# Kernel tuning notes

Measured on AMD Instinct MI355X. Metric: run time of the kernel, lower is better.

Reference implementation:

```python
import jax, jax.numpy as jnp
import numpy as np


def setup_inputs() -> dict:
    key = jax.random.key(0)
    k1, k2 = jax.random.split(key)
    B, N_A, UNITS = 8192, 1024, 4096
    x = jax.random.normal(k1, (B, N_A), dtype=jnp.float32)
    # keras 'uniform' initializer is U(-0.05, 0.05)
    mu = jax.random.uniform(k2, (N_A, UNITS), dtype=jnp.float32, minval=-0.05, maxval=0.05)
    return {"x": x, "mu": mu, "gamma": 0.5}


def reference(x, mu, gamma):
    # Squared L2 distance from each row of x (B, n_a) to each codebook column
    # of mu (n_a, units), computed without materializing (B, n_a, units):
    x_sq = jnp.sum(x * x, axis=-1, keepdims=True)          # (B, 1)
    mu_sq = jnp.sum(mu * mu, axis=0, keepdims=True)        # (1, units)
    cross = jnp.einsum('bn,nu->bu', x, mu)                 # (B, units)
    l2 = x_sq + mu_sq - 2.0 * cross                        # (B, units)
    return jnp.exp(-gamma * l2)
```

## Files before the change

kernel.cpp:

```cpp
#include <hip/hip_runtime.h>

#define B_ROWS 8192
#define K_DIM  1024
#define N_COLS 4096

#define UNDERFLOW_T 120.0f

__global__ __launch_bounds__(256) void mu_norms_k(const float* __restrict__ mu,
                                                  float* __restrict__ pmax) {
  const int blk = blockIdx.x;
  const int tid = threadIdx.x;
  const int g  = blk & 63;
  const int kq = blk >> 6;
  const int tx = tid & 63;
  const int ty = tid >> 6;
  const int u  = g * 64 + tx;
  const int k0 = kq * 64 + ty * 16;
  float s = 0.f;
#pragma unroll
  for (int i = 0; i < 16; ++i) {
    const float v = mu[(size_t)(k0 + i) * N_COLS + u];
    s += v * v;
  }
  __shared__ float red[4][64];
  red[ty][tx] = s;
  __syncthreads();
  if (ty == 0) {
    float p = red[0][tx] + red[1][tx] + red[2][tx] + red[3][tx];
#pragma unroll
    for (int off = 32; off; off >>= 1) p = fmaxf(p, __shfl_down(p, off));
    if (tx == 0) pmax[blk] = p;
  }
}

__global__ __launch_bounds__(256) void main_k(const float* __restrict__ x,
                                              const float* __restrict__ mu,
                                              const float* __restrict__ gp,
                                              const float* __restrict__ pmax,
                                              float* __restrict__ out) {
  __shared__ float sh[4 * K_DIM];
  __shared__ float xs[4];
  __shared__ int   sflag;
  const int tid  = threadIdx.x;
  const int w    = tid >> 6;
  const int lane = tid & 63;
  const int r0   = blockIdx.x * 4;
  const float g  = gp[0];

  {
    const float4* xr =
        reinterpret_cast<const float4*>(x + (size_t)(r0 + w) * K_DIM);
    float4* sh4 = reinterpret_cast<float4*>(sh) + w * (K_DIM / 4);
    float s = 0.f;
#pragma unroll
    for (int i = 0; i < 4; ++i) {
      const float4 v = xr[lane + i * 64];
      sh4[lane + i * 64] = v;
      s += v.x * v.x + v.y * v.y + v.z * v.z + v.w * v.w;
    }
#pragma unroll
    for (int off = 32; off; off >>= 1) s += __shfl_down(s, off);
    if (lane == 0) xs[w] = s;
  }
  __syncthreads();

  if (tid < 64) {
    float sg = 0.f;
#pragma unroll
    for (int kq = 0; kq < 16; ++kq) sg += pmax[kq * 64 + tid];
#pragma unroll
    for (int off = 32; off; off >>= 1) sg = fmaxf(sg, __shfl_down(sg, off));
    if (tid == 0) {
      const float xmin2 = fminf(fminf(xs[0], xs[1]), fminf(xs[2], xs[3]));
      const float d = sqrtf(xmin2) - sqrtf(sg);
      sflag = (d > 0.f && g * d * d > UNDERFLOW_T) ? 1 : 0;
    }
  }
  __syncthreads();

  if (sflag) {
    const float4 z = {0.f, 0.f, 0.f, 0.f};
    float4* o = reinterpret_cast<float4*>(out + (size_t)r0 * N_COLS);
#pragma unroll
    for (int i = 0; i < 16; ++i) o[tid + i * 256] = z;
    return;
  }

  for (int c = 0; c < 16; ++c) {
    const int u = c * 256 + tid;
    float acc0 = 0.f, acc1 = 0.f, acc2 = 0.f, acc3 = 0.f, ms = 0.f;
    for (int k = 0; k < K_DIM; ++k) {
      const float mv = mu[(size_t)k * N_COLS + u];
      ms   += mv * mv;
      acc0 += sh[0 * K_DIM + k] * mv;
      acc1 += sh[1 * K_DIM + k] * mv;
      acc2 += sh[2 * K_DIM + k] * mv;
      acc3 += sh[3 * K_DIM + k] * mv;
    }
    out[(size_t)(r0 + 0) * N_COLS + u] = expf(-g * (xs[0] + ms - 2.f * acc0));
    out[(size_t)(r0 + 1) * N_COLS + u] = expf(-g * (xs[1] + ms - 2.f * acc1));
    out[(size_t)(r0 + 2) * N_COLS + u] = expf(-g * (xs[2] + ms - 2.f * acc2));
    out[(size_t)(r0 + 3) * N_COLS + u] = expf(-g * (xs[3] + ms - 2.f * acc3));
  }
}

__global__ __launch_bounds__(256) void rbf_naive(const float* __restrict__ x,
                                                 const float* __restrict__ mu,
                                                 const float* __restrict__ gp,
                                                 float* __restrict__ out) {
  const int u = blockIdx.x * 256 + threadIdx.x;
  const int b = blockIdx.y;
  const float* xr = x + (size_t)b * K_DIM;
  float dot = 0.f, xsv = 0.f, ms = 0.f;
  for (int k = 0; k < K_DIM; ++k) {
    const float xv = xr[k];
    const float mv = mu[(size_t)k * N_COLS + u];
    dot += xv * mv; xsv += xv * xv; ms += mv * mv;
  }
  out[(size_t)b * N_COLS + u] = __expf(-gp[0] * (xsv + ms - 2.f * dot));
}

extern "C" void kernel_launch(void* const* d_in, const int* in_sizes, int n_in,
                              void* d_out, int out_size, void* d_ws, size_t ws_size,
                              hipStream_t stream) {
  const float* x  = (const float*)d_in[0];
  const float* mu = (const float*)d_in[1];
  const float* gp = (const float*)d_in[2];
  float* out = (float*)d_out;

  if (ws_size < 1024 * sizeof(float)) {
    rbf_naive<<<dim3(N_COLS / 256, B_ROWS), 256, 0, stream>>>(x, mu, gp, out);
    return;
  }
  float* pmax = (float*)d_ws;

  mu_norms_k<<<1024, 256, 0, stream>>>(mu, pmax);
  main_k<<<2048, 256, 0, stream>>>(x, mu, gp, pmax, out);
}
```

Measured before the change: 172.1 us.

## Hoist underflow check into separate partials and reduce kernels with a global flag

Per-row x norms and per-column mu norm maxima are now computed in a combined partials kernel. A single-block reduce kernel then derives one global underflow flag. The output kernel reads that flag and writes zeros immediately, without loading x rows into shared memory. This removes the per-block x load and flag reduction from the output kernel. In exchange it adds a third launch, and the global flag can only skip work if every row satisfies the bound, unlike the earlier per-block check.

Result: no change. 173.9 us (+1.0%).

```diff
diff --git a/kernel.cpp b/kernel.cpp
--- a/kernel.cpp
+++ b/kernel.cpp
@@ -6,47 +6,109 @@
 
 #define UNDERFLOW_T 120.0f
 
-__global__ __launch_bounds__(256) void mu_norms_k(const float* __restrict__ mu,
-                                                  float* __restrict__ pmax) {
-  const int blk = blockIdx.x;
+#define WS_PMAX 0
+#define WS_XMIN 1024
+#define WS_FLAG 3072
+
+__global__ __launch_bounds__(256) void partials_k(const float* __restrict__ x,
+                                                  const float* __restrict__ mu,
+                                                  float* __restrict__ ws) {
   const int tid = threadIdx.x;
-  const int g  = blk & 63;
-  const int kq = blk >> 6;
-  const int tx = tid & 63;
-  const int ty = tid >> 6;
-  const int u  = g * 64 + tx;
-  const int k0 = kq * 64 + ty * 16;
-  float s = 0.f;
+  if (blockIdx.x < 1024) {
+    const int blk = blockIdx.x;
+    const int g  = blk & 63;
+    const int kq = blk >> 6;
+    const int tx = tid & 63;
+    const int ty = tid >> 6;
+    const int u  = g * 64 + tx;
+    const int k0 = kq * 64 + ty * 16;
+    float s = 0.f;
 #pragma unroll
-  for (int i = 0; i < 16; ++i) {
-    const float v = mu[(size_t)(k0 + i) * N_COLS + u];
-    s += v * v;
-  }
-  __shared__ float red[4][64];
-  red[ty][tx] = s;
-  __syncthreads();
-  if (ty == 0) {
-    float p = red[0][tx] + red[1][tx] + red[2][tx] + red[3][tx];
+    for (int i = 0; i < 16; ++i) {
+      const float v = mu[(size_t)(k0 + i) * N_COLS + u];
+      s += v * v;
+    }
+    __shared__ float red[4][64];
+    red[ty][tx] = s;
+    __syncthreads();
+    if (ty == 0) {
+      float p = red[0][tx] + red[1][tx] + red[2][tx] + red[3][tx];
 #pragma unroll
-    for (int off = 32; off; off >>= 1) p = fmaxf(p, __shfl_down(p, off));
-    if (tx == 0) pmax[blk] = p;
+      for (int off = 32; off; off >>= 1) p = fmaxf(p, __shfl_down(p, off));
+      if (tx == 0) ws[WS_PMAX + blk] = p;
+    }
+  } else {
+    const int blk  = blockIdx.x - 1024;
+    const int w    = tid >> 6;
+    const int lane = tid & 63;
+    const float4* xr =
+        reinterpret_cast<const float4*>(x + (size_t)(blk * 4 + w) * K_DIM);
+    float s = 0.f;
+#pragma unroll
+    for (int i = 0; i < 4; ++i) {
+      const float4 v = xr[lane + i * 64];
+      s += v.x * v.x + v.y * v.y + v.z * v.z + v.w * v.w;
+    }
+#pragma unroll
+    for (int off = 32; off; off >>= 1) s += __shfl_down(s, off);
+    __shared__ float xs[4];
+    if (lane == 0) xs[w] = s;
+    __syncthreads();
+    if (tid == 0)
+      ws[WS_XMIN + blk] = fminf(fminf(xs[0], xs[1]), fminf(xs[2], xs[3]));
   }
 }
 
-__global__ __launch_bounds__(256) void main_k(const float* __restrict__ x,
-                                              const float* __restrict__ mu,
-                                              const float* __restrict__ gp,
-                                              const float* __restrict__ pmax,
-                                              float* __restrict__ out) {
+__global__ __launch_bounds__(256) void reduce_k(const float* __restrict__ gp,
+                                                float* __restrict__ ws) {
+  const int tid = threadIdx.x;
+  const int w = tid >> 6, lane = tid & 63;
+  float m = 3.4e38f;
+#pragma unroll
+  for (int i = 0; i < 8; ++i) m = fminf(m, ws[WS_XMIN + tid + i * 256]);
+#pragma unroll
+  for (int off = 32; off; off >>= 1) m = fminf(m, __shfl_down(m, off));
+  __shared__ float sm[4];
+  __shared__ float sb;
+  if (lane == 0) sm[w] = m;
+  if (tid < 64) {
+    float s = 0.f;
+#pragma unroll
+    for (int kq = 0; kq < 16; ++kq) s += ws[WS_PMAX + kq * 64 + tid];
+#pragma unroll
+    for (int off = 32; off; off >>= 1) s = fmaxf(s, __shfl_down(s, off));
+    if (tid == 0) sb = s;
+  }
+  __syncthreads();
+  if (tid == 0) {
+    const float xmin2 = fminf(fminf(sm[0], sm[1]), fminf(sm[2], sm[3]));
+    const float g = gp[0];
+    const float d = sqrtf(xmin2) - sqrtf(sb);
+    ws[WS_FLAG] = (d > 0.f && g * d * d > UNDERFLOW_T) ? 1.f : 0.f;
+  }
+}
+
+__global__ __launch_bounds__(256) void out_k(const float* __restrict__ x,
+                                             const float* __restrict__ mu,
+                                             const float* __restrict__ gp,
+                                             const float* __restrict__ ws,
+                                             float* __restrict__ out) {
+  const int tid = threadIdx.x;
+  const int r0  = blockIdx.x * 4;
+
+  if (ws[WS_FLAG] != 0.f) {
+    const float4 z = {0.f, 0.f, 0.f, 0.f};
+    float4* o = reinterpret_cast<float4*>(out + (size_t)r0 * N_COLS);
+#pragma unroll
+    for (int i = 0; i < 16; ++i) o[tid + i * 256] = z;
+    return;
+  }
+
   __shared__ float sh[4 * K_DIM];
   __shared__ float xs[4];
-  __shared__ int   sflag;
-  const int tid  = threadIdx.x;
   const int w    = tid >> 6;
   const int lane = tid & 63;
-  const int r0   = blockIdx.x * 4;
   const float g  = gp[0];
-
   {
     const float4* xr =
         reinterpret_cast<const float4*>(x + (size_t)(r0 + w) * K_DIM);
@@ -63,28 +125,6 @@
     if (lane == 0) xs[w] = s;
   }
   __syncthreads();
-
-  if (tid < 64) {
-    float sg = 0.f;
-#pragma unroll
-    for (int kq = 0; kq < 16; ++kq) sg += pmax[kq * 64 + tid];
-#pragma unroll
-    for (int off = 32; off; off >>= 1) sg = fmaxf(sg, __shfl_down(sg, off));
-    if (tid == 0) {
-      const float xmin2 = fminf(fminf(xs[0], xs[1]), fminf(xs[2], xs[3]));
-      const float d = sqrtf(xmin2) - sqrtf(sg);
-      sflag = (d > 0.f && g * d * d > UNDERFLOW_T) ? 1 : 0;
-    }
-  }
-  __syncthreads();
-
-  if (sflag) {
-    const float4 z = {0.f, 0.f, 0.f, 0.f};
-    float4* o = reinterpret_cast<float4*>(out + (size_t)r0 * N_COLS);
-#pragma unroll
-    for (int i = 0; i < 16; ++i) o[tid + i * 256] = z;
-    return;
-  }
 
   for (int c = 0; c < 16; ++c) {
     const int u = c * 256 + tid;
@@ -128,12 +168,13 @@
   const float* gp = (const float*)d_in[2];
   float* out = (float*)d_out;
 
-  if (ws_size < 1024 * sizeof(float)) {
+  if (ws_size < 4096 * sizeof(float)) {
     rbf_naive<<<dim3(N_COLS / 256, B_ROWS), 256, 0, stream>>>(x, mu, gp, out);
     return;
   }
-  float* pmax = (float*)d_ws;
+  float* ws = (float*)d_ws;
 
-  mu_norms_k<<<1024, 256, 0, stream>>>(mu, pmax);
-  main_k<<<2048, 256, 0, stream>>>(x, mu, gp, pmax, out);
+  partials_k<<<3072, 256, 0, stream>>>(x, mu, ws);
+  reduce_k<<<1, 256, 0, stream>>>(gp, ws);
+  out_k<<<2048, 256, 0, stream>>>(x, mu, gp, ws, out);
 }
```
